# Performance work log

Hardware: AMD Instinct MI355X
Metric: run time of the kernel (lower is better)

## Reference

```python
import jax, jax.numpy as jnp
from jax import lax
import numpy as np

INPUT_SIZE = 256
HIDDEN = 256


def _gru_scan(x, W_ih, W_hh, b_ih, b_hh):
    # x: [b, t, in], PyTorch GRU gate order: r, z, n
    b, t, _ = x.shape
    k = W_hh.shape[1]
    # precompute input contribution for all timesteps: [b, t, 3k]
    gx = jnp.einsum('bti,gi->btg', x, W_ih) + b_ih

    def step(h, gxt):
        gh = h @ W_hh.T + b_hh                 # [b, 3k]
        xr, xz, xn = jnp.split(gxt, 3, axis=-1)
        hr, hz, hn = jnp.split(gh, 3, axis=-1)
        r = jax.nn.sigmoid(xr + hr)
        z = jax.nn.sigmoid(xz + hz)
        n = jnp.tanh(xn + r * hn)
        h_new = (1.0 - z) * n + z * h
        return h_new, h_new

    h0 = jnp.zeros((b, k), x.dtype)
    _, hs = lax.scan(step, h0, jnp.swapaxes(gx, 0, 1))  # hs: [t, b, k]
    return hs


def setup_inputs() -> dict:
    key = jax.random.key(0)
    kx, k1, k2, k3, k4 = jax.random.split(key, 5)
    s_ih = 1.0 / np.sqrt(HIDDEN)
    x = jax.random.normal(kx, (32, 2048, INPUT_SIZE), dtype=jnp.float32)
    W_ih = jax.random.uniform(k1, (3 * HIDDEN, INPUT_SIZE), jnp.float32, -s_ih, s_ih)
    W_hh = jax.random.uniform(k2, (3 * HIDDEN, HIDDEN), jnp.float32, -s_ih, s_ih)
    b_ih = jax.random.uniform(k3, (3 * HIDDEN,), jnp.float32, -s_ih, s_ih)
    b_hh = jax.random.uniform(k4, (3 * HIDDEN,), jnp.float32, -s_ih, s_ih)
    return {'x': x, 'W_ih': W_ih, 'W_hh': W_hh, 'b_ih': b_ih, 'b_hh': b_hh}


def reference(x, W_ih, W_hh, b_ih, b_hh):
    # forward direction
    hs_f = _gru_scan(x, W_ih, W_hh, b_ih, b_hh)                     # [t, b, k]
    # 'bidirectional': same weights applied to time-reversed input
    hs_r = _gru_scan(x[:, ::-1, :], W_ih, W_hh, b_ih, b_hh)[::-1]   # [t, b, k]
    outputs = jnp.concatenate(
        (jnp.swapaxes(hs_f, 0, 1), jnp.swapaxes(hs_r, 0, 1)), axis=2)  # [b, t, 2k]
    hiddens = jnp.concatenate((hs_f, hs_r), axis=2)                    # [t, b, 2k]
    return outputs, hiddens
```

## Files before the change

kernel.cpp:

```cpp
#include <hip/hip_runtime.h>
#include <hip/hip_fp16.h>


typedef __fp16 half2_t __attribute__((ext_vector_type(2)));
typedef __fp16 half8_t __attribute__((ext_vector_type(8)));
typedef float  f32x4   __attribute__((ext_vector_type(4)));

static constexpr int T_STEPS = 2048;
static constexpr int BATCH   = 32;
static constexpr int HID     = 256;
static constexpr int IN      = 256;
static constexpr int G3      = 768;

__device__ __forceinline__ float fdot2(half2_t a, half2_t b, float c) {
    return __builtin_amdgcn_fdot2(a, b, c, false);
}

__device__ __forceinline__ void barrier_lgkm() {
    asm volatile("s_waitcnt lgkmcnt(0)\n\ts_barrier" ::: "memory");
}

__global__ __launch_bounds__(256, 2) void gx_gemm(
        const float* __restrict__ x,
        const float* __restrict__ Wih,
        const float* __restrict__ bih,
        const float* __restrict__ bhh,
        _Float16* __restrict__ gx) {
    __shared__ ushort As[64 * 256];
    __shared__ ushort Bs[64 * 256];

    const int tid = threadIdx.x;
    const int m0  = blockIdx.x * 64;
    const int tx  = tid & 15;
    const int ty  = tid >> 4;

#pragma unroll
    for (int i = 0; i < 16; ++i) {
        int f    = tid + 256 * i;
        int row  = f >> 6;
        int col4 = f & 63;
        float4 v = *(const float4*)(x + (size_t)(m0 + row) * IN + col4 * 4);
        half2_t h0 = __builtin_amdgcn_cvt_pkrtz(v.x, v.y);
        half2_t h1 = __builtin_amdgcn_cvt_pkrtz(v.z, v.w);
        int chunk = col4 >> 1;
        int idx = row * 256 + ((chunk ^ (row & 7)) * 8) + (col4 & 1) * 4;
        uint2 wv;
        wv.x = __builtin_bit_cast(unsigned, h0);
        wv.y = __builtin_bit_cast(unsigned, h1);
        *(uint2*)(As + idx) = wv;
    }

    for (int nb = 0; nb < 12; ++nb) {
#pragma unroll
        for (int i = 0; i < 16; ++i) {
            int f    = tid + 256 * i;
            int row  = f >> 6;
            int col4 = f & 63;
            float4 v = *(const float4*)(Wih + (size_t)(nb * 64 + row) * IN + col4 * 4);
            half2_t h0 = __builtin_amdgcn_cvt_pkrtz(v.x, v.y);
            half2_t h1 = __builtin_amdgcn_cvt_pkrtz(v.z, v.w);
            int chunk = col4 >> 1;
            int idx = row * 256 + ((chunk ^ (row & 7)) * 8) + (col4 & 1) * 4;
            uint2 wv;
            wv.x = __builtin_bit_cast(unsigned, h0);
            wv.y = __builtin_bit_cast(unsigned, h1);
            *(uint2*)(Bs + idx) = wv;
        }
        barrier_lgkm();

        float acc[4][4];
#pragma unroll
        for (int jm = 0; jm < 4; ++jm)
#pragma unroll
            for (int jn = 0; jn < 4; ++jn) acc[jm][jn] = 0.f;

#pragma unroll 4
        for (int kc = 0; kc < 32; ++kc) {
            union { uint4 u; half2_t h[4]; } av[4], bv[4];
#pragma unroll
            for (int jm = 0; jm < 4; ++jm) {
                int r = ty * 4 + jm;
                av[jm].u = *(const uint4*)(As + r * 256 + ((kc ^ (r & 7)) * 8));
            }
#pragma unroll
            for (int jn = 0; jn < 4; ++jn) {
                int r = tx + 16 * jn;
                bv[jn].u = *(const uint4*)(Bs + r * 256 + ((kc ^ (r & 7)) * 8));
            }
#pragma unroll
            for (int jm = 0; jm < 4; ++jm)
#pragma unroll
                for (int jn = 0; jn < 4; ++jn)
#pragma unroll
                    for (int p = 0; p < 4; ++p)
                        acc[jm][jn] = fdot2(av[jm].h[p], bv[jn].h[p], acc[jm][jn]);
        }

#pragma unroll
        for (int jn = 0; jn < 4; ++jn) {
            int n = nb * 64 + tx + 16 * jn;
            float bias = bih[n] + (n < 512 ? bhh[n] : 0.f);
#pragma unroll
            for (int jm = 0; jm < 4; ++jm) {
                int m = m0 + ty * 4 + jm;
                gx[(size_t)m * G3 + n] = (_Float16)(acc[jm][jn] + bias);
            }
        }
        barrier_lgkm();
    }
}

__global__ __launch_bounds__(512) void gru_seq(
        const _Float16* __restrict__ gx,
        const float* __restrict__ Whh,
        const float* __restrict__ bhh,
        float* __restrict__ out0,
        float* __restrict__ out1) {
    __shared__ float  ghM[384];
    __shared__ float  PV[2][384];
    __shared__ ushort h16[256];
    __shared__ ushort gxb[768];

    const int tid = threadIdx.x;
    const int b   = blockIdx.x & 31;
    const int d   = blockIdx.x >> 5;
    const int w   = tid >> 6;
    const int L   = tid & 63;

    const int tp0 = d ? (T_STEPS - 1) : 0;
    const int sgn = d ? -1 : 1;

    if (tid < 256) h16[tid] = 0;
    __syncthreads();

    if (w < 4) {
        const int i    = tid;
        const int khf  = i >> 7;
        const int r0   = 3 * (i & 127);

        half2_t Wv[3][64];
#pragma unroll
        for (int j = 0; j < 3; ++j) {
            const float* wr_ = Whh + (size_t)(384 + r0 + j) * HID + khf * 128;
#pragma unroll
            for (int q = 0; q < 64; ++q) {
                float2 f = *(const float2*)(wr_ + 2 * q);
                Wv[j][q] = __builtin_amdgcn_cvt_pkrtz(f.x, f.y);
            }
        }

        float bh_n  = bhh[512 + i];
        float hprev = 0.f;

        float* o0 = out0 + ((size_t)b * T_STEPS + tp0) * 512 + d * 256 + i;
        float* o1 = out1 + ((size_t)tp0 * BATCH + b) * 512 + d * 256 + i;
        const int o0d = sgn * 512;
        const int o1d = sgn * (BATCH * 512);

        const ushort* hbase = h16 + khf * 128;
        const _Float16* gxh = (const _Float16*)gxb;

        for (int t = 0; t < T_STEPS; ++t) {
            float a0 = 0.f, a1 = 0.f, a2 = 0.f;
#pragma unroll
            for (int hc = 0; hc < 4; ++hc) {
                union { uint4 u; half2_t h[4]; } hv[4];
#pragma unroll
                for (int c = 0; c < 4; ++c)
                    hv[c].u = *(const uint4*)(hbase + hc * 32 + c * 8);
#pragma unroll
                for (int c = 0; c < 4; ++c)
#pragma unroll
                    for (int p = 0; p < 4; ++p) {
                        const int q = hc * 16 + c * 4 + p;
                        a0 = fdot2(Wv[0][q], hv[c].h[p], a0);
                        a1 = fdot2(Wv[1][q], hv[c].h[p], a1);
                        a2 = fdot2(Wv[2][q], hv[c].h[p], a2);
                    }
            }
            PV[khf][r0 + 0] = a0;
            PV[khf][r0 + 1] = a1;
            PV[khf][r0 + 2] = a2;

            barrier_lgkm();

            float hr = ghM[i];
            float hz = (i < 128) ? ghM[256 + i]
                                 : (PV[0][i - 128] + PV[1][i - 128]);
            float hn = PV[0][128 + i] + PV[1][128 + i];
            float xr = (float)gxh[i]       + hr;
            float xz = (float)gxh[256 + i] + hz;
            float r = __builtin_amdgcn_rcpf(1.f + __builtin_amdgcn_exp2f(xr * -1.44269504f));
            float z = __builtin_amdgcn_rcpf(1.f + __builtin_amdgcn_exp2f(xz * -1.44269504f));
            float nx = (float)gxh[512 + i] + r * (hn + bh_n);
            float e2 = __builtin_amdgcn_exp2f(nx * 2.88539008f);
            float n  = 1.f - 2.f * __builtin_amdgcn_rcpf(1.f + e2);
            float h  = n + z * (hprev - n);
            hprev = h;

            h16[i] = __builtin_bit_cast(ushort, (_Float16)h);
            *o0 = h; *o1 = h;
            o0 += o0d; o1 += o1d;

            barrier_lgkm();
        }
    } else {
        const int mw = w - 4;
        half8_t Wn[6][8];
        {
            const int mrow = L & 15;
            const int klo  = (L >> 4) * 8;
#pragma unroll
            for (int nt = 0; nt < 6; ++nt)
#pragma unroll
                for (int kh = 0; kh < 8; ++kh) {
                    const float* p = Whh + (size_t)((6 * mw + nt) * 16 + mrow) * HID
                                   + kh * 32 + klo;
                    union { half8_t v; half2_t h[4]; } u;
#pragma unroll
                    for (int q = 0; q < 4; ++q) {
                        float2 f = *(const float2*)(p + 2 * q);
                        u.h[q] = __builtin_amdgcn_cvt_pkrtz(f.x, f.y);
                    }
                    Wn[nt][kh] = u.v;
                }
        }

        const int pt = tid - 256;
        const bool pf = pt < 96;
        const _Float16* gp = gx + ((size_t)b * T_STEPS + tp0) * G3 + (pf ? pt * 8 : 0);
        const int gpd = sgn * G3;
        uint4 greg{};
        if (pf) greg = *(const uint4*)gp;

        const ushort* hseg = h16 + (L >> 4) * 8;
        float* pw0 = ghM + (L >> 4) * 4;
        const bool wr = (L & 15) == 0;

        for (int t = 0; t < T_STEPS; ++t) {
            if (pf) {
                *(uint4*)(gxb + pt * 8) = greg;
                if (t + 1 < T_STEPS) {
                    gp += gpd;
                    greg = *(const uint4*)gp;
                }
            }

            union { uint4 u; half8_t v; } bf[8];
#pragma unroll
            for (int kh = 0; kh < 8; ++kh)
                bf[kh].u = *(const uint4*)(hseg + kh * 32);

#pragma unroll
            for (int nt = 0; nt < 6; ++nt) {
                f32x4 zz = {0.f, 0.f, 0.f, 0.f};
                f32x4 accA = __builtin_amdgcn_mfma_f32_16x16x32_f16(Wn[nt][0], bf[0].v, zz, 0, 0, 0);
                f32x4 accB = __builtin_amdgcn_mfma_f32_16x16x32_f16(Wn[nt][4], bf[4].v, zz, 0, 0, 0);
                accA = __builtin_amdgcn_mfma_f32_16x16x32_f16(Wn[nt][1], bf[1].v, accA, 0, 0, 0);
                accB = __builtin_amdgcn_mfma_f32_16x16x32_f16(Wn[nt][5], bf[5].v, accB, 0, 0, 0);
                accA = __builtin_amdgcn_mfma_f32_16x16x32_f16(Wn[nt][2], bf[2].v, accA, 0, 0, 0);
                accB = __builtin_amdgcn_mfma_f32_16x16x32_f16(Wn[nt][6], bf[6].v, accB, 0, 0, 0);
                accA = __builtin_amdgcn_mfma_f32_16x16x32_f16(Wn[nt][3], bf[3].v, accA, 0, 0, 0);
                accB = __builtin_amdgcn_mfma_f32_16x16x32_f16(Wn[nt][7], bf[7].v, accB, 0, 0, 0);
                if (wr) {
                    f32x4 s = accA + accB;
                    *(f32x4*)(pw0 + (6 * mw + nt) * 16) = s;
                }
            }

            barrier_lgkm();
            barrier_lgkm();
        }
    }
}

extern "C" void kernel_launch(void* const* d_in, const int* in_sizes, int n_in,
                              void* d_out, int out_size, void* d_ws, size_t ws_size,
                              hipStream_t stream) {
    const float* x   = (const float*)d_in[0];
    const float* Wih = (const float*)d_in[1];
    const float* Whh = (const float*)d_in[2];
    const float* bih = (const float*)d_in[3];
    const float* bhh = (const float*)d_in[4];

    float* out0 = (float*)d_out;
    float* out1 = out0 + (size_t)BATCH * T_STEPS * 512;

    _Float16* gx = (_Float16*)d_ws;

    gx_gemm<<<dim3(65536 / 64), dim3(256), 0, stream>>>(x, Wih, bih, bhh, gx);
    gru_seq<<<dim3(BATCH * 2), dim3(512), 0, stream>>>(gx, Whh, bhh, out0, out1);
}
```

Before: 2.560 ms.

## Double recurrent-kernel block to 1024 threads, splitting K four ways across waves

Grows the per-sequence block from 8 to 16 waves. The fdot2 waves now split the hidden dimension four ways instead of two, and the MFMA waves each handle 3 tiles instead of 6. This halves the per-wave serial dot-product and MFMA chain length on the latency-bound recurrent step. In exchange, the elementwise gate work now runs on only a quarter of the fdot2 threads, there are extra partial-sum reads, and barriers cover twice as many waves.

```diff
diff --git a/kernel.cpp b/kernel.cpp
--- a/kernel.cpp
+++ b/kernel.cpp
@@ -110,14 +110,14 @@
     }
 }
 
-__global__ __launch_bounds__(512) void gru_seq(
+__global__ __launch_bounds__(1024) void gru_seq(
         const _Float16* __restrict__ gx,
         const float* __restrict__ Whh,
         const float* __restrict__ bhh,
         float* __restrict__ out0,
         float* __restrict__ out1) {
     __shared__ float  ghM[384];
-    __shared__ float  PV[2][384];
+    __shared__ float  PV[4][384];
     __shared__ ushort h16[256];
     __shared__ ushort gxb[768];
 
@@ -133,88 +133,93 @@
     if (tid < 256) h16[tid] = 0;
     __syncthreads();
 
-    if (w < 4) {
-        const int i    = tid;
-        const int khf  = i >> 7;
-        const int r0   = 3 * (i & 127);
-
-        half2_t Wv[3][64];
+    if (w < 8) {
+        const int s  = w & 3;
+        const int g  = w >> 2;
+        const int r0 = g * 192 + 3 * L;
+
+        half2_t Wv[3][32];
 #pragma unroll
         for (int j = 0; j < 3; ++j) {
-            const float* wr_ = Whh + (size_t)(384 + r0 + j) * HID + khf * 128;
-#pragma unroll
-            for (int q = 0; q < 64; ++q) {
+            const float* wr_ = Whh + (size_t)(384 + r0 + j) * HID + s * 64;
+#pragma unroll
+            for (int q = 0; q < 32; ++q) {
                 float2 f = *(const float2*)(wr_ + 2 * q);
                 Wv[j][q] = __builtin_amdgcn_cvt_pkrtz(f.x, f.y);
             }
         }
 
-        float bh_n  = bhh[512 + i];
-        float hprev = 0.f;
-
-        float* o0 = out0 + ((size_t)b * T_STEPS + tp0) * 512 + d * 256 + i;
-        float* o1 = out1 + ((size_t)tp0 * BATCH + b) * 512 + d * 256 + i;
+        float bh_n = 0.f, hprev = 0.f;
+        float* o0 = out0;
+        float* o1 = out1;
+        if (tid < 256) {
+            bh_n = bhh[512 + tid];
+            o0 = out0 + ((size_t)b * T_STEPS + tp0) * 512 + d * 256 + tid;
+            o1 = out1 + ((size_t)tp0 * BATCH + b) * 512 + d * 256 + tid;
+        }
         const int o0d = sgn * 512;
         const int o1d = sgn * (BATCH * 512);
 
-        const ushort* hbase = h16 + khf * 128;
+        const ushort* hq = h16 + s * 64;
         const _Float16* gxh = (const _Float16*)gxb;
 
         for (int t = 0; t < T_STEPS; ++t) {
+            union { uint4 u; half2_t h[4]; } hv[8];
+#pragma unroll
+            for (int c = 0; c < 8; ++c)
+                hv[c].u = *(const uint4*)(hq + c * 8);
+
             float a0 = 0.f, a1 = 0.f, a2 = 0.f;
 #pragma unroll
-            for (int hc = 0; hc < 4; ++hc) {
-                union { uint4 u; half2_t h[4]; } hv[4];
-#pragma unroll
-                for (int c = 0; c < 4; ++c)
-                    hv[c].u = *(const uint4*)(hbase + hc * 32 + c * 8);
-#pragma unroll
-                for (int c = 0; c < 4; ++c)
-#pragma unroll
-                    for (int p = 0; p < 4; ++p) {
-                        const int q = hc * 16 + c * 4 + p;
-                        a0 = fdot2(Wv[0][q], hv[c].h[p], a0);
-                        a1 = fdot2(Wv[1][q], hv[c].h[p], a1);
-                        a2 = fdot2(Wv[2][q], hv[c].h[p], a2);
-                    }
-            }
-            PV[khf][r0 + 0] = a0;
-            PV[khf][r0 + 1] = a1;
-            PV[khf][r0 + 2] = a2;
-
-            barrier_lgkm();
-
-            float hr = ghM[i];
-            float hz = (i < 128) ? ghM[256 + i]
-                                 : (PV[0][i - 128] + PV[1][i - 128]);
-            float hn = PV[0][128 + i] + PV[1][128 + i];
-            float xr = (float)gxh[i]       + hr;
-            float xz = (float)gxh[256 + i] + hz;
-            float r = __builtin_amdgcn_rcpf(1.f + __builtin_amdgcn_exp2f(xr * -1.44269504f));
-            float z = __builtin_amdgcn_rcpf(1.f + __builtin_amdgcn_exp2f(xz * -1.44269504f));
-            float nx = (float)gxh[512 + i] + r * (hn + bh_n);
-            float e2 = __builtin_amdgcn_exp2f(nx * 2.88539008f);
-            float n  = 1.f - 2.f * __builtin_amdgcn_rcpf(1.f + e2);
-            float h  = n + z * (hprev - n);
-            hprev = h;
-
-            h16[i] = __builtin_bit_cast(ushort, (_Float16)h);
-            *o0 = h; *o1 = h;
-            o0 += o0d; o1 += o1d;
-
+            for (int c = 0; c < 8; ++c)
+#pragma unroll
+                for (int p = 0; p < 4; ++p) {
+                    const int q = c * 4 + p;
+                    a0 = fdot2(Wv[0][q], hv[c].h[p], a0);
+                    a1 = fdot2(Wv[1][q], hv[c].h[p], a1);
+                    a2 = fdot2(Wv[2][q], hv[c].h[p], a2);
+                }
+            PV[s][r0 + 0] = a0;
+            PV[s][r0 + 1] = a1;
+            PV[s][r0 + 2] = a2;
+
+            barrier_lgkm();
+
+            if (tid < 256) {
+                const int i = tid;
+                float hr = ghM[i];
+                float hz = (i < 128) ? ghM[256 + i]
+                                     : ((PV[0][i - 128] + PV[1][i - 128])
+                                      + (PV[2][i - 128] + PV[3][i - 128]));
+                float hn = (PV[0][128 + i] + PV[1][128 + i])
+                         + (PV[2][128 + i] + PV[3][128 + i]);
+                float xr = (float)gxh[i]       + hr;
+                float xz = (float)gxh[256 + i] + hz;
+                float r = __builtin_amdgcn_rcpf(1.f + __builtin_amdgcn_exp2f(xr * -1.44269504f));
+                float z = __builtin_amdgcn_rcpf(1.f + __builtin_amdgcn_exp2f(xz * -1.44269504f));
+                float nx = (float)gxh[512 + i] + r * (hn + bh_n);
+                float e2 = __builtin_amdgcn_exp2f(nx * 2.88539008f);
+                float n  = 1.f - 2.f * __builtin_amdgcn_rcpf(1.f + e2);
+                float h  = n + z * (hprev - n);
+                hprev = h;
+
+                h16[i] = __builtin_bit_cast(ushort, (_Float16)h);
+                *o0 = h; *o1 = h;
+                o0 += o0d; o1 += o1d;
+            }
             barrier_lgkm();
         }
     } else {
-        const int mw = w - 4;
-        half8_t Wn[6][8];
+        const int mw = w - 8;
+        half8_t Wn[3][8];
         {
             const int mrow = L & 15;
             const int klo  = (L >> 4) * 8;
 #pragma unroll
-            for (int nt = 0; nt < 6; ++nt)
+            for (int nt = 0; nt < 3; ++nt)
 #pragma unroll
                 for (int kh = 0; kh < 8; ++kh) {
-                    const float* p = Whh + (size_t)((6 * mw + nt) * 16 + mrow) * HID
+                    const float* p = Whh + (size_t)(48 * mw + nt * 16 + mrow) * HID
                                    + kh * 32 + klo;
                     union { half8_t v; half2_t h[4]; } u;
 #pragma unroll
@@ -226,8 +231,8 @@
                 }
         }
 
-        const int pt = tid - 256;
-        const bool pf = pt < 96;
+        const int pt = tid - 768;
+        const bool pf = (unsigned)pt < 96u;
         const _Float16* gp = gx + ((size_t)b * T_STEPS + tp0) * G3 + (pf ? pt * 8 : 0);
         const int gpd = sgn * G3;
         uint4 greg{};
@@ -252,7 +257,7 @@
                 bf[kh].u = *(const uint4*)(hseg + kh * 32);
 
 #pragma unroll
-            for (int nt = 0; nt < 6; ++nt) {
+            for (int nt = 0; nt < 3; ++nt) {
                 f32x4 zz = {0.f, 0.f, 0.f, 0.f};
                 f32x4 accA = __builtin_amdgcn_mfma_f32_16x16x32_f16(Wn[nt][0], bf[0].v, zz, 0, 0, 0);
                 f32x4 accB = __builtin_amdgcn_mfma_f32_16x16x32_f16(Wn[nt][4], bf[4].v, zz, 0, 0, 0);
@@ -263,8 +268,8 @@
                 accA = __builtin_amdgcn_mfma_f32_16x16x32_f16(Wn[nt][3], bf[3].v, accA, 0, 0, 0);
                 accB = __builtin_amdgcn_mfma_f32_16x16x32_f16(Wn[nt][7], bf[7].v, accB, 0, 0, 0);
                 if (wr) {
-                    f32x4 s = accA + accB;
-                    *(f32x4*)(pw0 + (6 * mw + nt) * 16) = s;
+                    f32x4 sm = accA + accB;
+                    *(f32x4*)(pw0 + (3 * mw + nt) * 16) = sm;
                 }
             }
 
@@ -289,5 +294,5 @@
     _Float16* gx = (_Float16*)d_ws;
 
     gx_gemm<<<dim3(65536 / 64), dim3(256), 0, stream>>>(x, Wih, bih, bhh, gx);
-    gru_seq<<<dim3(BATCH * 2), dim3(512), 0, stream>>>(gx, Whh, bhh, out0, out1);
-}
+    gru_seq<<<dim3(BATCH * 2), dim3(1024), 0, stream>>>(gx, Whh, bhh, out0, out1);
+}
```

New measurement: 4.223 ms. +65.0%, slower.
